# Kernel optimization log

Hardware: AMD Instinct MI355X
Metric: run time of the kernel (lower is better)

The kernel has to match this reference:

```python
import jax, jax.numpy as jnp
import numpy as np

B, S, E = 2, 2048, 1024
D_ATTN, H = 1024, 16
HD = D_ATTN // H
SCALE = 1.0 / np.sqrt(D_ATTN)
ROPE_BASE = 10000.0


def setup_inputs() -> dict:
    key = jax.random.key(0)
    ks = jax.random.split(key, 7)
    def w(k, shape, scale):
        return jax.random.normal(k, shape, dtype=jnp.float32) * scale
    return {
        "q": w(ks[0], (B, S, E), 1.0),
        "k": w(ks[1], (B, S, E), 1.0),
        "v": w(ks[2], (B, S, E), 1.0),
        "Wq": w(ks[3], (D_ATTN, E), E ** -0.5),
        "Wk": w(ks[4], (D_ATTN, E), E ** -0.5),
        "Wv": w(ks[5], (D_ATTN, E), E ** -0.5),
        "Wo": w(ks[6], (E, D_ATTN), D_ATTN ** -0.5),
    }


def _rope(x):
    # x: [B, H, S, HD]; interleaved-pair rotary embedding over the seq axis
    s, d = x.shape[2], x.shape[3]
    half = d // 2
    inv_freq = 1.0 / (ROPE_BASE ** (jnp.arange(half, dtype=jnp.float32) * 2.0 / d))
    ang = jnp.arange(s, dtype=jnp.float32)[:, None] * inv_freq[None, :]  # [S, half]
    cos, sin = jnp.cos(ang), jnp.sin(ang)
    xr = x.reshape(x.shape[:-1] + (half, 2))
    x0, x1 = xr[..., 0], xr[..., 1]
    o0 = x0 * cos - x1 * sin
    o1 = x0 * sin + x1 * cos
    return jnp.stack([o0, o1], axis=-1).reshape(x.shape)


def reference(q, k, v, Wq, Wk, Wv, Wo):
    # linear projections (nn.Linear with weight [out, in]): y = x @ W^T
    qh = (q @ Wq.T).reshape(B, S, H, HD).transpose(0, 2, 1, 3)  # [B,H,S,HD]
    kh = (k @ Wk.T).reshape(B, S, H, HD).transpose(0, 2, 1, 3)
    vh = (v @ Wv.T).reshape(B, S, H, HD).transpose(0, 2, 1, 3)
    qh = _rope(qh)
    kh = _rope(kh)
    # shifted-causal mask: disallow j >= i (diagonal masked), except (0,0) allowed
    i = jnp.arange(S)[:, None]
    j = jnp.arange(S)[None, :]
    masked = j >= i                              # triu incl. diagonal
    masked = masked.at[0, 0].set(False)          # keep (0,0) so row 0 isn't all -inf
    scores = jnp.einsum("bhsd,bhtd->bhst", qh, kh) * SCALE
    scores = jnp.where(masked, -jnp.inf, scores)
    probs = jax.nn.softmax(scores, axis=-1)      # dropout omitted (eval mode)
    ctx = jnp.einsum("bhst,bhtd->bhsd", probs, vh)
    ctx = ctx.transpose(0, 2, 1, 3).reshape(B, S, D_ATTN)
    return ctx @ Wo.T
```

## Files before the change

kernel.cpp:

```cpp
#include <hip/hip_runtime.h>
#include <hip/hip_bf16.h>

#define BATCH 2
#define SEQ   2048
#define EMB   1024
#define DATTN 1024
#define NH    16
#define HD    64
#define MM    (BATCH*SEQ)
#define SCALE 0.03125f
#define MINIT -1.0e30f
#define ROPE_COEF 0.41524101186f

using bf16x8 = __attribute__((ext_vector_type(8))) short;
using f32x4  = __attribute__((ext_vector_type(4))) float;

__device__ inline short f2bf(float x) {
    __hip_bfloat16 b = __float2bfloat16(x);
    return *reinterpret_cast<short*>(&b);
}

__device__ inline void gl_lds16(const short* g, short* l) {
    __builtin_amdgcn_global_load_lds(
        (const __attribute__((address_space(1))) unsigned int*)g,
        (__attribute__((address_space(3))) unsigned int*)l, 16, 0, 0);
}

__global__ __launch_bounds__(256)
void cvt_all(const float* __restrict__ q, const float* __restrict__ k,
             const float* __restrict__ v,
             const float* __restrict__ Wq, const float* __restrict__ Wk,
             const float* __restrict__ Wv, const float* __restrict__ Wo,
             short* __restrict__ dst)
{
    const long QKV = (long)MM * EMB;
    const long WSZ = (long)DATTN * EMB;
    const long i = ((long)blockIdx.x * 256 + threadIdx.x) * 4;
    const float* s;
    long off;
    if (i < 3 * QKV) {
        const int seg = (int)(i / QKV);
        off = i - (long)seg * QKV;
        s = (seg == 0) ? q : (seg == 1) ? k : v;
    } else {
        const long j = i - 3 * QKV;
        const int seg = (int)(j / WSZ);
        off = j - (long)seg * WSZ;
        s = (seg == 0) ? Wq : (seg == 1) ? Wk : (seg == 2) ? Wv : Wo;
    }
    float4 x = *(const float4*)(s + off);
    short4 y;
    y.x = f2bf(x.x); y.y = f2bf(x.y); y.z = f2bf(x.z); y.w = f2bf(x.w);
    *(short4*)(dst + i) = y;
}

__device__ inline void stage_tile64(const short* g, short* lds, int tid) {
    #pragma unroll
    for (int c = 0; c < 4; ++c) {
        const int cc   = c * 256 + tid;
        const int row  = cc >> 3;
        const int slot = cc & 7;
        const int ssl  = slot ^ (row & 7);
        gl_lds16(g + (long)row * EMB + ssl * 8, lds + ((cc & ~63) << 3));
    }
}

__device__ inline void stage_tile64h(const short* g, short* lds, int tid) {
    #pragma unroll
    for (int c = 0; c < 2; ++c) {
        const int cc   = c * 256 + tid;
        const int row  = cc >> 3;
        const int ssl  = (cc & 7) ^ (row & 7);
        gl_lds16(g + (long)row * EMB + ssl * 8, lds + ((cc & ~63) << 3));
    }
}

__global__ __launch_bounds__(256)
void gemm_proj_bf16(const short* __restrict__ qb, const short* __restrict__ kb,
                    const short* __restrict__ vb,
                    const short* __restrict__ wqb, const short* __restrict__ wkb,
                    const short* __restrict__ wvb,
                    short* __restrict__ Qb, short* __restrict__ Kb,
                    short* __restrict__ Vtb)
{
    const short* A; const short* B;
    if (blockIdx.z == 0)      { A = qb; B = wqb; }
    else if (blockIdx.z == 1) { A = kb; B = wkb; }
    else                      { A = vb; B = wvb; }
    const bool isv = (blockIdx.z == 2);

    __shared__ short sA[128 * 64];
    __shared__ short sB[128 * 64];

    const int tid  = threadIdx.x;
    const int wave = tid >> 6, lane = tid & 63;
    const int quad = lane >> 4, l16 = lane & 15;
    const int wm = (wave >> 1) * 64, wn = (wave & 1) * 64;
    const long m0 = (long)blockIdx.x * 128, n0 = (long)blockIdx.y * 128;
    const int rsw = l16 & 7;

    f32x4 acc[4][4];
    #pragma unroll
    for (int i = 0; i < 4; ++i)
        #pragma unroll
        for (int j = 0; j < 4; ++j) acc[i][j] = (f32x4){0.f, 0.f, 0.f, 0.f};

    for (int kt = 0; kt < EMB; kt += 64) {
        __syncthreads();
        stage_tile64(A + m0 * EMB + kt, sA, tid);
        stage_tile64(B + n0 * EMB + kt, sB, tid);
        __syncthreads();

        #pragma unroll
        for (int kk = 0; kk < 2; ++kk) {
            bf16x8 af[4], bfr[4];
            #pragma unroll
            for (int rt = 0; rt < 4; ++rt)
                af[rt] = *(const bf16x8*)&sA[(wm + rt * 16 + l16) * 64
                         + (((kk << 2) | quad) ^ rsw) * 8];
            #pragma unroll
            for (int ct = 0; ct < 4; ++ct)
                bfr[ct] = *(const bf16x8*)&sB[(wn + ct * 16 + l16) * 64
                          + (((kk << 2) | quad) ^ rsw) * 8];
            if (isv) {
                #pragma unroll
                for (int i = 0; i < 4; ++i)
                    #pragma unroll
                    for (int j = 0; j < 4; ++j)
                        acc[i][j] = __builtin_amdgcn_mfma_f32_16x16x32_bf16(
                            af[i], bfr[j], acc[i][j], 0, 0, 0);
            } else {
                #pragma unroll
                for (int i = 0; i < 4; ++i)
                    #pragma unroll
                    for (int j = 0; j < 4; ++j)
                        acc[i][j] = __builtin_amdgcn_mfma_f32_16x16x32_bf16(
                            bfr[i], af[j], acc[i][j], 0, 0, 0);
            }
        }
    }

    if (!isv) {
        short* C = (blockIdx.z == 0) ? Qb : Kb;
        const float scl = (blockIdx.z == 0) ? SCALE : 1.0f;
        #pragma unroll
        for (int i = 0; i < 4; ++i) {
            const int d0  = (int)(n0) + wn + i * 16 + quad * 4;
            const int hh  = d0 >> 6, dd0 = d0 & (HD - 1);
            const float invf0 = exp2f(-ROPE_COEF * (float)(dd0 >> 1));
            const float invf1 = exp2f(-ROPE_COEF * (float)((dd0 >> 1) + 1));
            #pragma unroll
            for (int j = 0; j < 4; ++j) {
                const int tok = (int)(m0) + wm + j * 16 + l16;
                const int bb = tok >> 11, ss = tok & (SEQ - 1);
                float s0, c0, s1, c1;
                __sincosf((float)ss * invf0, &s0, &c0);
                __sincosf((float)ss * invf1, &s1, &c1);
                const f32x4 x = acc[i][j];
                short4 o4;
                o4.x = f2bf((x[0] * c0 - x[1] * s0) * scl);
                o4.y = f2bf((x[0] * s0 + x[1] * c0) * scl);
                o4.z = f2bf((x[2] * c1 - x[3] * s1) * scl);
                o4.w = f2bf((x[2] * s1 + x[3] * c1) * scl);
                *(short4*)&C[(((long)(bb * NH + hh)) << 17)
                             + ((long)ss << 6) + dd0] = o4;
            }
        }
    } else {
        #pragma unroll
        for (int rt = 0; rt < 4; ++rt) {
            #pragma unroll
            for (int ct = 0; ct < 4; ++ct) {
                const long row0 = m0 + wm + rt * 16 + quad * 4;
                const long col  = n0 + wn + ct * 16 + l16;
                const int bb = (int)(row0 >> 11), ss = (int)(row0 & (SEQ - 1));
                const int hh = (int)(col >> 6),   dd = (int)(col & (HD - 1));
                short4 s4;
                s4.x = f2bf(acc[rt][ct][0]); s4.y = f2bf(acc[rt][ct][1]);
                s4.z = f2bf(acc[rt][ct][2]); s4.w = f2bf(acc[rt][ct][3]);
                *(short4*)&Vtb[(((long)(bb * NH + hh)) << 17) + ((long)dd << 11) + ss] = s4;
            }
        }
    }
}

__global__ __launch_bounds__(256)
void gemm_out_bf16(const short* __restrict__ Ab, const short* __restrict__ Bb,
                   float* __restrict__ C)
{
    __shared__ short sA[128 * 64];
    __shared__ short sB[64 * 64];

    const int tid  = threadIdx.x;
    const int wave = tid >> 6, lane = tid & 63;
    const int quad = lane >> 4, l16 = lane & 15;
    const int wm = (wave >> 1) * 64, wn = (wave & 1) * 32;
    const long m0 = (long)blockIdx.x * 128, n0 = (long)blockIdx.y * 64;
    const int rsw = l16 & 7;

    f32x4 acc[4][2];
    #pragma unroll
    for (int i = 0; i < 4; ++i)
        #pragma unroll
        for (int j = 0; j < 2; ++j) acc[i][j] = (f32x4){0.f, 0.f, 0.f, 0.f};

    for (int kt = 0; kt < DATTN; kt += 64) {
        __syncthreads();
        stage_tile64(Ab + m0 * DATTN + kt, sA, tid);
        stage_tile64h(Bb + n0 * DATTN + kt, sB, tid);
        __syncthreads();

        #pragma unroll
        for (int kk = 0; kk < 2; ++kk) {
            bf16x8 af[4], bfr[2];
            #pragma unroll
            for (int rt = 0; rt < 4; ++rt)
                af[rt] = *(const bf16x8*)&sA[(wm + rt * 16 + l16) * 64
                         + (((kk << 2) | quad) ^ rsw) * 8];
            #pragma unroll
            for (int ct = 0; ct < 2; ++ct)
                bfr[ct] = *(const bf16x8*)&sB[(wn + ct * 16 + l16) * 64
                          + (((kk << 2) | quad) ^ rsw) * 8];
            #pragma unroll
            for (int rt = 0; rt < 4; ++rt)
                #pragma unroll
                for (int ct = 0; ct < 2; ++ct)
                    acc[rt][ct] = __builtin_amdgcn_mfma_f32_16x16x32_bf16(
                        af[rt], bfr[ct], acc[rt][ct], 0, 0, 0);
        }
    }

    #pragma unroll
    for (int rt = 0; rt < 4; ++rt) {
        #pragma unroll
        for (int ct = 0; ct < 2; ++ct) {
            #pragma unroll
            for (int reg = 0; reg < 4; ++reg) {
                const long row = m0 + wm + rt * 16 + quad * 4 + reg;
                const long col = n0 + wn + ct * 16 + l16;
                C[row * EMB + col] = acc[rt][ct][reg];
            }
        }
    }
}

#define KLD 64
#define PLD 72

__device__ inline void stage_kv64(const short* __restrict__ Kb,
                                  const short* __restrict__ Vtb,
                                  long base, int jb2,
                                  short* skp, short* svp,
                                  int tid, int wave)
{
    #pragma unroll
    for (int c = 0; c < 2; ++c) {
        const int cc  = c * 256 + tid;
        const int row = cc >> 3;
        const int sch = (cc & 7) ^ (row & 7);
        short* dk = skp + ((c * 256 + (tid & ~63)) << 3) - ((tid & ~63) << 3)
                        + (((c * 256 + tid) & ~63) - (c * 256 + tid - (tid & 63)) ) ;
        (void)dk;
        gl_lds16(Kb + base + (long)(jb2 + row) * HD + sch * 8,
                 skp + ((c * 256 + wave * 64) << 3));
        gl_lds16(Vtb + base + ((long)row << 11) + jb2 + sch * 8,
                 svp + ((c * 256 + wave * 64) << 3));
    }
}

__global__ __launch_bounds__(256, 3)
void flash_attn_mfma(const short* __restrict__ Qb,
                     const short* __restrict__ Kb,
                     const short* __restrict__ Vtb,
                     short* __restrict__ ctx)
{
    const int id  = blockIdx.x;
    const int hi  = id >> 8;
    const int idx = id & 255;
    const int r   = idx & 7;
    const int s5  = idx >> 3;
    const int pi  = s5 & 3;
    const int ts8 = s5 >> 2;
    const int p   = r + 8 * pi;
    const int b   = p >> 4, h = p & 15;
    const int t   = hi ? ts8 : (15 - ts8);

    const int tid = threadIdx.x;
    const int wave = tid >> 6, lane = tid & 63;
    const int quad = lane >> 4, l16 = lane & 15;
    const int r0 = t * 128;

    __shared__ short sk[2][64 * KLD];
    __shared__ short sv[2][64 * KLD];
    __shared__ short sp[4][32 * PLD];

    const long base = ((long)(b * NH + h)) << 17;

    const int iq0 = r0 + wave * 32 + l16;
    const int iq1 = iq0 + 16;
    const int dtile = 2 * t + (wave >> 1);
    const int rsw = l16 & 7;

    bf16x8 qf0[2], qf1[2];
    #pragma unroll
    for (int tt = 0; tt < 2; ++tt) {
        qf0[tt] = *(const bf16x8*)(Qb + base + (long)iq0 * HD + tt * 32 + quad * 8);
        qf1[tt] = *(const bf16x8*)(Qb + base + (long)iq1 * HD + tt * 32 + quad * 8);
    }

    f32x4 acc0[4], acc1[4];
    #pragma unroll
    for (int ct = 0; ct < 4; ++ct) {
        acc0[ct] = (f32x4){0.f, 0.f, 0.f, 0.f};
        acc1[ct] = (f32x4){0.f, 0.f, 0.f, 0.f};
    }
    float m0 = MINIT, l0 = 0.f;
    float m1 = MINIT, l1 = 0.f;

    const int J = 2 * t + 2;

    stage_kv64(Kb, Vtb, base, 0, sk[0], sv[0], tid, wave);

    #pragma unroll 1
    for (int j2 = 0; j2 < J; ++j2) {
        const int pb = j2 & 1;
        asm volatile("s_waitcnt vmcnt(0)" ::: "memory");
        __builtin_amdgcn_s_barrier();
        if (j2 + 1 < J)
            stage_kv64(Kb, Vtb, base, (j2 + 1) * 64,
                       sk[pb ^ 1], sv[pb ^ 1], tid, wave);

        if (j2 <= dtile) {
            const int jb2 = j2 * 64;
            const short* skh = sk[pb];
            const short* svh = sv[pb];

            f32x4 s0[4], s1[4];
            __builtin_amdgcn_s_setprio(1);
            #pragma unroll
            for (int ct = 0; ct < 4; ++ct) {
                const int rr16 = (ct * 16 + l16) * KLD;
                bf16x8 k0 = *(const bf16x8*)&skh[rr16 + ((quad ^ rsw) << 3)];
                bf16x8 k1 = *(const bf16x8*)&skh[rr16 + (((4 + quad) ^ rsw) << 3)];
                f32x4 z0 = (f32x4){0.f, 0.f, 0.f, 0.f};
                z0 = __builtin_amdgcn_mfma_f32_16x16x32_bf16(k0, qf0[0], z0, 0, 0, 0);
                z0 = __builtin_amdgcn_mfma_f32_16x16x32_bf16(k1, qf0[1], z0, 0, 0, 0);
                s0[ct] = z0;
                f32x4 z1 = (f32x4){0.f, 0.f, 0.f, 0.f};
                z1 = __builtin_amdgcn_mfma_f32_16x16x32_bf16(k0, qf1[0], z1, 0, 0, 0);
                z1 = __builtin_amdgcn_mfma_f32_16x16x32_bf16(k1, qf1[1], z1, 0, 0, 0);
                s1[ct] = z1;
            }
            __builtin_amdgcn_s_setprio(0);

            if (j2 == dtile) {
                #pragma unroll
                for (int ct = 0; ct < 4; ++ct)
                    #pragma unroll
                    for (int rr = 0; rr < 4; ++rr) {
                        const int j = jb2 + ct * 16 + quad * 4 + rr;
                        if (!((j < iq0) || (iq0 == 0 && j == 0)))
                            s0[ct][rr] = -INFINITY;
                        if (!(j < iq1))
                            s1[ct][rr] = -INFINITY;
                    }
            }

            float mx0 = MINIT;
            #pragma unroll
            for (int ct = 0; ct < 4; ++ct)
                #pragma unroll
                for (int rr = 0; rr < 4; ++rr) mx0 = fmaxf(mx0, s0[ct][rr]);
            mx0 = fmaxf(mx0, __shfl_xor(mx0, 16, 64));
            mx0 = fmaxf(mx0, __shfl_xor(mx0, 32, 64));
            const float mn0 = fmaxf(m0, mx0);
            const float a0 = __expf(m0 - mn0);
            m0 = mn0;
            float ss0 = 0.f;
            #pragma unroll
            for (int ct = 0; ct < 4; ++ct)
                #pragma unroll
                for (int rr = 0; rr < 4; ++rr) {
                    const float e = __expf(s0[ct][rr] - mn0);
                    s0[ct][rr] = e;
                    ss0 += e;
                }
            ss0 += __shfl_xor(ss0, 16, 64);
            ss0 += __shfl_xor(ss0, 32, 64);
            l0 = l0 * a0 + ss0;

            float mx1 = MINIT;
            #pragma unroll
            for (int ct = 0; ct < 4; ++ct)
                #pragma unroll
                for (int rr = 0; rr < 4; ++rr) mx1 = fmaxf(mx1, s1[ct][rr]);
            mx1 = fmaxf(mx1, __shfl_xor(mx1, 16, 64));
            mx1 = fmaxf(mx1, __shfl_xor(mx1, 32, 64));
            const float mn1 = fmaxf(m1, mx1);
            const float a1 = __expf(m1 - mn1);
            m1 = mn1;
            float ss1 = 0.f;
            #pragma unroll
            for (int ct = 0; ct < 4; ++ct)
                #pragma unroll
                for (int rr = 0; rr < 4; ++rr) {
                    const float e = __expf(s1[ct][rr] - mn1);
                    s1[ct][rr] = e;
                    ss1 += e;
                }
            ss1 += __shfl_xor(ss1, 16, 64);
            ss1 += __shfl_xor(ss1, 32, 64);
            l1 = l1 * a1 + ss1;

            short* pw0 = sp[wave];
            short* pw1 = sp[wave] + 16 * PLD;
            #pragma unroll
            for (int ct = 0; ct < 4; ++ct) {
                short4 p4;
                p4.x = f2bf(s0[ct][0]); p4.y = f2bf(s0[ct][1]);
                p4.z = f2bf(s0[ct][2]); p4.w = f2bf(s0[ct][3]);
                *(short4*)&pw0[l16 * PLD + ct * 16 + quad * 4] = p4;
                short4 q4;
                q4.x = f2bf(s1[ct][0]); q4.y = f2bf(s1[ct][1]);
                q4.z = f2bf(s1[ct][2]); q4.w = f2bf(s1[ct][3]);
                *(short4*)&pw1[l16 * PLD + ct * 16 + quad * 4] = q4;
            }

            #pragma unroll
            for (int ct = 0; ct < 4; ++ct)
                #pragma unroll
                for (int rr = 0; rr < 4; ++rr) {
                    acc0[ct][rr] *= a0;
                    acc1[ct][rr] *= a1;
                }

            bf16x8 pf00 = *(const bf16x8*)&pw0[l16 * PLD + quad * 8];
            bf16x8 pf01 = *(const bf16x8*)&pw0[l16 * PLD + 32 + quad * 8];
            bf16x8 pf10 = *(const bf16x8*)&pw1[l16 * PLD + quad * 8];
            bf16x8 pf11 = *(const bf16x8*)&pw1[l16 * PLD + 32 + quad * 8];

            __builtin_amdgcn_s_setprio(1);
            #pragma unroll
            for (int ct = 0; ct < 4; ++ct) {
                const int rr16 = (ct * 16 + l16) * KLD;
                bf16x8 v0 = *(const bf16x8*)&svh[rr16 + ((quad ^ rsw) << 3)];
                bf16x8 v1 = *(const bf16x8*)&svh[rr16 + (((4 + quad) ^ rsw) << 3)];
                acc0[ct] = __builtin_amdgcn_mfma_f32_16x16x32_bf16(
                    v0, pf00, acc0[ct], 0, 0, 0);
                acc0[ct] = __builtin_amdgcn_mfma_f32_16x16x32_bf16(
                    v1, pf01, acc0[ct], 0, 0, 0);
                acc1[ct] = __builtin_amdgcn_mfma_f32_16x16x32_bf16(
                    v0, pf10, acc1[ct], 0, 0, 0);
                acc1[ct] = __builtin_amdgcn_mfma_f32_16x16x32_bf16(
                    v1, pf11, acc1[ct], 0, 0, 0);
            }
            __builtin_amdgcn_s_setprio(0);
        }
    }

    {
        const float inv0 = 1.f / l0;
        short* orow = ctx + (long)(b * SEQ + iq0) * DATTN + h * HD;
        #pragma unroll
        for (int ct = 0; ct < 4; ++ct) {
            short4 o4;
            o4.x = f2bf(acc0[ct][0] * inv0);
            o4.y = f2bf(acc0[ct][1] * inv0);
            o4.z = f2bf(acc0[ct][2] * inv0);
            o4.w = f2bf(acc0[ct][3] * inv0);
            *(short4*)&orow[ct * 16 + quad * 4] = o4;
        }
    }
    {
        const float inv1 = 1.f / l1;
        short* orow = ctx + (long)(b * SEQ + iq1) * DATTN + h * HD;
        #pragma unroll
        for (int ct = 0; ct < 4; ++ct) {
            short4 o4;
            o4.x = f2bf(acc1[ct][0] * inv1);
            o4.y = f2bf(acc1[ct][1] * inv1);
            o4.z = f2bf(acc1[ct][2] * inv1);
            o4.w = f2bf(acc1[ct][3] * inv1);
            *(short4*)&orow[ct * 16 + quad * 4] = o4;
        }
    }
}

extern "C" void kernel_launch(void* const* d_in, const int* in_sizes, int n_in,
                              void* d_out, int out_size, void* d_ws, size_t ws_size,
                              hipStream_t stream) {
    const float* q  = (const float*)d_in[0];
    const float* k  = (const float*)d_in[1];
    const float* v  = (const float*)d_in[2];
    const float* Wq = (const float*)d_in[3];
    const float* Wk = (const float*)d_in[4];
    const float* Wv = (const float*)d_in[5];
    const float* Wo = (const float*)d_in[6];
    float* out = (float*)d_out;

    const long QKV = (long)MM * EMB;
    const long WSZ = (long)DATTN * EMB;
    short* basep = (short*)d_ws;
    short* qb  = basep;
    short* kb  = qb + QKV;
    short* vb  = kb + QKV;
    short* wqb = vb + QKV;
    short* wkb = wqb + WSZ;
    short* wvb = wkb + WSZ;
    short* wob = wvb + WSZ;
    short* Qb  = wob + WSZ;
    short* Kb  = Qb + QKV;
    short* Vtb = Kb + QKV;
    short* ctx = Vtb + QKV;

    cvt_all<<<16384, 256, 0, stream>>>(q, k, v, Wq, Wk, Wv, Wo, qb);

    gemm_proj_bf16<<<dim3(MM / 128, DATTN / 128, 3), 256, 0, stream>>>(
        qb, kb, vb, wqb, wkb, wvb, Qb, Kb, Vtb);

    flash_attn_mfma<<<512, 256, 0, stream>>>(Qb, Kb, Vtb, ctx);

    gemm_out_bf16<<<dim3(MM / 128, EMB / 64), 256, 0, stream>>>(ctx, wob, out);
}
```

Baseline: 211.0 us.

## Load K/V straight to registers in flash attention with smaller 64-row blocks

The flash-attention kernel no longer stages K and V tiles through double-buffered shared memory with barriers. Each wave now loads its K/V MFMA fragments directly from global memory into registers. Blocks shrink to 128 threads covering 64 query rows, and the grid doubles to 1024 with a new load-balancing order for causal tile lengths. This removes LDS staging and block-wide barriers, and the finer grid should balance the causal workload better. In exchange, both waves of a block fetch the same K/V from global memory or L2 with no reuse, and the loads are no longer prefetched a tile ahead.

```diff
diff --git a/kernel.cpp b/kernel.cpp
--- a/kernel.cpp
+++ b/kernel.cpp
@@ -244,62 +244,38 @@
     }
 }
 
-#define KLD 64
 #define PLD 72
 
-__device__ inline void stage_kv64(const short* __restrict__ Kb,
-                                  const short* __restrict__ Vtb,
-                                  long base, int jb2,
-                                  short* skp, short* svp,
-                                  int tid, int wave)
-{
-    #pragma unroll
-    for (int c = 0; c < 2; ++c) {
-        const int cc  = c * 256 + tid;
-        const int row = cc >> 3;
-        const int sch = (cc & 7) ^ (row & 7);
-        short* dk = skp + ((c * 256 + (tid & ~63)) << 3) - ((tid & ~63) << 3)
-                        + (((c * 256 + tid) & ~63) - (c * 256 + tid - (tid & 63)) ) ;
-        (void)dk;
-        gl_lds16(Kb + base + (long)(jb2 + row) * HD + sch * 8,
-                 skp + ((c * 256 + wave * 64) << 3));
-        gl_lds16(Vtb + base + ((long)row << 11) + jb2 + sch * 8,
-                 svp + ((c * 256 + wave * 64) << 3));
-    }
-}
-
-__global__ __launch_bounds__(256, 3)
+__global__ __launch_bounds__(128, 2)
 void flash_attn_mfma(const short* __restrict__ Qb,
                      const short* __restrict__ Kb,
                      const short* __restrict__ Vtb,
                      short* __restrict__ ctx)
 {
-    const int id  = blockIdx.x;
-    const int hi  = id >> 8;
-    const int idx = id & 255;
-    const int r   = idx & 7;
-    const int s5  = idx >> 3;
-    const int pi  = s5 & 3;
-    const int ts8 = s5 >> 2;
-    const int p   = r + 8 * pi;
-    const int b   = p >> 4, h = p & 15;
-    const int t   = hi ? ts8 : (15 - ts8);
-
-    const int tid = threadIdx.x;
+    const int id = blockIdx.x;
+    const int r  = id & 7;
+    const int pi = (id >> 3) & 3;
+    const int us = id >> 5;
+    const int p  = r + 8 * pi;
+    const int b  = p >> 4, h = p & 15;
+    int u;
+    if      (us < 8)  u = 31 - us;
+    else if (us < 16) u = us - 8;
+    else if (us < 24) u = 39 - us;
+    else              u = us - 16;
+
+    const int tid  = threadIdx.x;
     const int wave = tid >> 6, lane = tid & 63;
     const int quad = lane >> 4, l16 = lane & 15;
-    const int r0 = t * 128;
-
-    __shared__ short sk[2][64 * KLD];
-    __shared__ short sv[2][64 * KLD];
-    __shared__ short sp[4][32 * PLD];
+
+    __shared__ short sp[2][32 * PLD];
 
     const long base = ((long)(b * NH + h)) << 17;
-
-    const int iq0 = r0 + wave * 32 + l16;
+    const short* __restrict__ kb = Kb + base;
+    const short* __restrict__ vb = Vtb + base;
+
+    const int iq0 = u * 64 + wave * 32 + l16;
     const int iq1 = iq0 + 16;
-    const int dtile = 2 * t + (wave >> 1);
-    const int rsw = l16 & 7;
 
     bf16x8 qf0[2], qf1[2];
     #pragma unroll
@@ -317,145 +293,137 @@
     float m0 = MINIT, l0 = 0.f;
     float m1 = MINIT, l1 = 0.f;
 
-    const int J = 2 * t + 2;
-
-    stage_kv64(Kb, Vtb, base, 0, sk[0], sv[0], tid, wave);
+    const int J = u + 1;
 
     #pragma unroll 1
     for (int j2 = 0; j2 < J; ++j2) {
-        const int pb = j2 & 1;
-        asm volatile("s_waitcnt vmcnt(0)" ::: "memory");
-        __builtin_amdgcn_s_barrier();
-        if (j2 + 1 < J)
-            stage_kv64(Kb, Vtb, base, (j2 + 1) * 64,
-                       sk[pb ^ 1], sv[pb ^ 1], tid, wave);
-
-        if (j2 <= dtile) {
-            const int jb2 = j2 * 64;
-            const short* skh = sk[pb];
-            const short* svh = sv[pb];
-
-            f32x4 s0[4], s1[4];
-            __builtin_amdgcn_s_setprio(1);
-            #pragma unroll
-            for (int ct = 0; ct < 4; ++ct) {
-                const int rr16 = (ct * 16 + l16) * KLD;
-                bf16x8 k0 = *(const bf16x8*)&skh[rr16 + ((quad ^ rsw) << 3)];
-                bf16x8 k1 = *(const bf16x8*)&skh[rr16 + (((4 + quad) ^ rsw) << 3)];
-                f32x4 z0 = (f32x4){0.f, 0.f, 0.f, 0.f};
-                z0 = __builtin_amdgcn_mfma_f32_16x16x32_bf16(k0, qf0[0], z0, 0, 0, 0);
-                z0 = __builtin_amdgcn_mfma_f32_16x16x32_bf16(k1, qf0[1], z0, 0, 0, 0);
-                s0[ct] = z0;
-                f32x4 z1 = (f32x4){0.f, 0.f, 0.f, 0.f};
-                z1 = __builtin_amdgcn_mfma_f32_16x16x32_bf16(k0, qf1[0], z1, 0, 0, 0);
-                z1 = __builtin_amdgcn_mfma_f32_16x16x32_bf16(k1, qf1[1], z1, 0, 0, 0);
-                s1[ct] = z1;
-            }
-            __builtin_amdgcn_s_setprio(0);
-
-            if (j2 == dtile) {
-                #pragma unroll
-                for (int ct = 0; ct < 4; ++ct)
-                    #pragma unroll
-                    for (int rr = 0; rr < 4; ++rr) {
-                        const int j = jb2 + ct * 16 + quad * 4 + rr;
-                        if (!((j < iq0) || (iq0 == 0 && j == 0)))
-                            s0[ct][rr] = -INFINITY;
-                        if (!(j < iq1))
-                            s1[ct][rr] = -INFINITY;
-                    }
-            }
-
-            float mx0 = MINIT;
-            #pragma unroll
-            for (int ct = 0; ct < 4; ++ct)
-                #pragma unroll
-                for (int rr = 0; rr < 4; ++rr) mx0 = fmaxf(mx0, s0[ct][rr]);
-            mx0 = fmaxf(mx0, __shfl_xor(mx0, 16, 64));
-            mx0 = fmaxf(mx0, __shfl_xor(mx0, 32, 64));
-            const float mn0 = fmaxf(m0, mx0);
-            const float a0 = __expf(m0 - mn0);
-            m0 = mn0;
-            float ss0 = 0.f;
+        const int jb2 = j2 * 64;
+
+        bf16x8 kf0[4], kf1[4], vf0[4], vf1[4];
+        #pragma unroll
+        for (int ct = 0; ct < 4; ++ct) {
+            const long krow = (long)(jb2 + ct * 16 + l16) * HD + quad * 8;
+            kf0[ct] = *(const bf16x8*)(kb + krow);
+            kf1[ct] = *(const bf16x8*)(kb + krow + 32);
+            const long vrow = ((long)(ct * 16 + l16) << 11) + jb2 + quad * 8;
+            vf0[ct] = *(const bf16x8*)(vb + vrow);
+            vf1[ct] = *(const bf16x8*)(vb + vrow + 32);
+        }
+
+        f32x4 s0[4], s1[4];
+        __builtin_amdgcn_s_setprio(1);
+        #pragma unroll
+        for (int ct = 0; ct < 4; ++ct) {
+            f32x4 z0 = (f32x4){0.f, 0.f, 0.f, 0.f};
+            z0 = __builtin_amdgcn_mfma_f32_16x16x32_bf16(kf0[ct], qf0[0], z0, 0, 0, 0);
+            z0 = __builtin_amdgcn_mfma_f32_16x16x32_bf16(kf1[ct], qf0[1], z0, 0, 0, 0);
+            s0[ct] = z0;
+            f32x4 z1 = (f32x4){0.f, 0.f, 0.f, 0.f};
+            z1 = __builtin_amdgcn_mfma_f32_16x16x32_bf16(kf0[ct], qf1[0], z1, 0, 0, 0);
+            z1 = __builtin_amdgcn_mfma_f32_16x16x32_bf16(kf1[ct], qf1[1], z1, 0, 0, 0);
+            s1[ct] = z1;
+        }
+        __builtin_amdgcn_s_setprio(0);
+
+        if (j2 == u) {
             #pragma unroll
             for (int ct = 0; ct < 4; ++ct)
                 #pragma unroll
                 for (int rr = 0; rr < 4; ++rr) {
-                    const float e = __expf(s0[ct][rr] - mn0);
-                    s0[ct][rr] = e;
-                    ss0 += e;
+                    const int j = jb2 + ct * 16 + quad * 4 + rr;
+                    if (!((j < iq0) || (iq0 == 0 && j == 0)))
+                        s0[ct][rr] = -INFINITY;
+                    if (!(j < iq1))
+                        s1[ct][rr] = -INFINITY;
                 }
-            ss0 += __shfl_xor(ss0, 16, 64);
-            ss0 += __shfl_xor(ss0, 32, 64);
-            l0 = l0 * a0 + ss0;
-
-            float mx1 = MINIT;
-            #pragma unroll
-            for (int ct = 0; ct < 4; ++ct)
-                #pragma unroll
-                for (int rr = 0; rr < 4; ++rr) mx1 = fmaxf(mx1, s1[ct][rr]);
-            mx1 = fmaxf(mx1, __shfl_xor(mx1, 16, 64));
-            mx1 = fmaxf(mx1, __shfl_xor(mx1, 32, 64));
-            const float mn1 = fmaxf(m1, mx1);
-            const float a1 = __expf(m1 - mn1);
-            m1 = mn1;
-            float ss1 = 0.f;
-            #pragma unroll
-            for (int ct = 0; ct < 4; ++ct)
-                #pragma unroll
-                for (int rr = 0; rr < 4; ++rr) {
-                    const float e = __expf(s1[ct][rr] - mn1);
-                    s1[ct][rr] = e;
-                    ss1 += e;
-                }
-            ss1 += __shfl_xor(ss1, 16, 64);
-            ss1 += __shfl_xor(ss1, 32, 64);
-            l1 = l1 * a1 + ss1;
-
-            short* pw0 = sp[wave];
-            short* pw1 = sp[wave] + 16 * PLD;
-            #pragma unroll
-            for (int ct = 0; ct < 4; ++ct) {
-                short4 p4;
-                p4.x = f2bf(s0[ct][0]); p4.y = f2bf(s0[ct][1]);
-                p4.z = f2bf(s0[ct][2]); p4.w = f2bf(s0[ct][3]);
-                *(short4*)&pw0[l16 * PLD + ct * 16 + quad * 4] = p4;
-                short4 q4;
-                q4.x = f2bf(s1[ct][0]); q4.y = f2bf(s1[ct][1]);
-                q4.z = f2bf(s1[ct][2]); q4.w = f2bf(s1[ct][3]);
-                *(short4*)&pw1[l16 * PLD + ct * 16 + quad * 4] = q4;
-            }
-
-            #pragma unroll
-            for (int ct = 0; ct < 4; ++ct)
-                #pragma unroll
-                for (int rr = 0; rr < 4; ++rr) {
-                    acc0[ct][rr] *= a0;
-                    acc1[ct][rr] *= a1;
-                }
-
-            bf16x8 pf00 = *(const bf16x8*)&pw0[l16 * PLD + quad * 8];
-            bf16x8 pf01 = *(const bf16x8*)&pw0[l16 * PLD + 32 + quad * 8];
-            bf16x8 pf10 = *(const bf16x8*)&pw1[l16 * PLD + quad * 8];
-            bf16x8 pf11 = *(const bf16x8*)&pw1[l16 * PLD + 32 + quad * 8];
-
-            __builtin_amdgcn_s_setprio(1);
-            #pragma unroll
-            for (int ct = 0; ct < 4; ++ct) {
-                const int rr16 = (ct * 16 + l16) * KLD;
-                bf16x8 v0 = *(const bf16x8*)&svh[rr16 + ((quad ^ rsw) << 3)];
-                bf16x8 v1 = *(const bf16x8*)&svh[rr16 + (((4 + quad) ^ rsw) << 3)];
-                acc0[ct] = __builtin_amdgcn_mfma_f32_16x16x32_bf16(
-                    v0, pf00, acc0[ct], 0, 0, 0);
-                acc0[ct] = __builtin_amdgcn_mfma_f32_16x16x32_bf16(
-                    v1, pf01, acc0[ct], 0, 0, 0);
-                acc1[ct] = __builtin_amdgcn_mfma_f32_16x16x32_bf16(
-                    v0, pf10, acc1[ct], 0, 0, 0);
-                acc1[ct] = __builtin_amdgcn_mfma_f32_16x16x32_bf16(
-                    v1, pf11, acc1[ct], 0, 0, 0);
-            }
-            __builtin_amdgcn_s_setprio(0);
-        }
+        }
+
+        float mx0 = MINIT;
+        #pragma unroll
+        for (int ct = 0; ct < 4; ++ct)
+            #pragma unroll
+            for (int rr = 0; rr < 4; ++rr) mx0 = fmaxf(mx0, s0[ct][rr]);
+        mx0 = fmaxf(mx0, __shfl_xor(mx0, 16, 64));
+        mx0 = fmaxf(mx0, __shfl_xor(mx0, 32, 64));
+        const float mn0 = fmaxf(m0, mx0);
+        const float a0 = __expf(m0 - mn0);
+        m0 = mn0;
+        float ss0 = 0.f;
+        #pragma unroll
+        for (int ct = 0; ct < 4; ++ct)
+            #pragma unroll
+            for (int rr = 0; rr < 4; ++rr) {
+                const float e = __expf(s0[ct][rr] - mn0);
+                s0[ct][rr] = e;
+                ss0 += e;
+            }
+        ss0 += __shfl_xor(ss0, 16, 64);
+        ss0 += __shfl_xor(ss0, 32, 64);
+        l0 = l0 * a0 + ss0;
+
+        float mx1 = MINIT;
+        #pragma unroll
+        for (int ct = 0; ct < 4; ++ct)
+            #pragma unroll
+            for (int rr = 0; rr < 4; ++rr) mx1 = fmaxf(mx1, s1[ct][rr]);
+        mx1 = fmaxf(mx1, __shfl_xor(mx1, 16, 64));
+        mx1 = fmaxf(mx1, __shfl_xor(mx1, 32, 64));
+        const float mn1 = fmaxf(m1, mx1);
+        const float a1 = __expf(m1 - mn1);
+        m1 = mn1;
+        float ss1 = 0.f;
+        #pragma unroll
+        for (int ct = 0; ct < 4; ++ct)
+            #pragma unroll
+            for (int rr = 0; rr < 4; ++rr) {
+                const float e = __expf(s1[ct][rr] - mn1);
+                s1[ct][rr] = e;
+                ss1 += e;
+            }
+        ss1 += __shfl_xor(ss1, 16, 64);
+        ss1 += __shfl_xor(ss1, 32, 64);
+        l1 = l1 * a1 + ss1;
+
+        short* pw0 = sp[wave];
+        short* pw1 = sp[wave] + 16 * PLD;
+        #pragma unroll
+        for (int ct = 0; ct < 4; ++ct) {
+            short4 p4;
+            p4.x = f2bf(s0[ct][0]); p4.y = f2bf(s0[ct][1]);
+            p4.z = f2bf(s0[ct][2]); p4.w = f2bf(s0[ct][3]);
+            *(short4*)&pw0[l16 * PLD + ct * 16 + quad * 4] = p4;
+            short4 q4;
+            q4.x = f2bf(s1[ct][0]); q4.y = f2bf(s1[ct][1]);
+            q4.z = f2bf(s1[ct][2]); q4.w = f2bf(s1[ct][3]);
+            *(short4*)&pw1[l16 * PLD + ct * 16 + quad * 4] = q4;
+        }
+
+        #pragma unroll
+        for (int ct = 0; ct < 4; ++ct)
+            #pragma unroll
+            for (int rr = 0; rr < 4; ++rr) {
+                acc0[ct][rr] *= a0;
+                acc1[ct][rr] *= a1;
+            }
+
+        bf16x8 pf00 = *(const bf16x8*)&pw0[l16 * PLD + quad * 8];
+        bf16x8 pf01 = *(const bf16x8*)&pw0[l16 * PLD + 32 + quad * 8];
+        bf16x8 pf10 = *(const bf16x8*)&pw1[l16 * PLD + quad * 8];
+        bf16x8 pf11 = *(const bf16x8*)&pw1[l16 * PLD + 32 + quad * 8];
+
+        __builtin_amdgcn_s_setprio(1);
+        #pragma unroll
+        for (int ct = 0; ct < 4; ++ct) {
+            acc0[ct] = __builtin_amdgcn_mfma_f32_16x16x32_bf16(
+                vf0[ct], pf00, acc0[ct], 0, 0, 0);
+            acc0[ct] = __builtin_amdgcn_mfma_f32_16x16x32_bf16(
+                vf1[ct], pf01, acc0[ct], 0, 0, 0);
+            acc1[ct] = __builtin_amdgcn_mfma_f32_16x16x32_bf16(
+                vf0[ct], pf10, acc1[ct], 0, 0, 0);
+            acc1[ct] = __builtin_amdgcn_mfma_f32_16x16x32_bf16(
+                vf1[ct], pf11, acc1[ct], 0, 0, 0);
+        }
+        __builtin_amdgcn_s_setprio(0);
     }
 
     {
@@ -518,7 +486,7 @@
     gemm_proj_bf16<<<dim3(MM / 128, DATTN / 128, 3), 256, 0, stream>>>(
         qb, kb, vb, wqb, wkb, wvb, Qb, Kb, Vtb);
 
-    flash_attn_mfma<<<512, 256, 0, stream>>>(Qb, Kb, Vtb, ctx);
+    flash_attn_mfma<<<1024, 128, 0, stream>>>(Qb, Kb, Vtb, ctx);
 
     gemm_out_bf16<<<dim3(MM / 128, EMB / 64), 256, 0, stream>>>(ctx, wob, out);
 }
```

Result: slower. 230.7 us (+9.3%).

## Use 128-wide KV tiles, exp2 softmax with folded log2e scale, lazy rescale

Applied to the files above, without the earlier changes.

Replaces the double-buffered 64-key KV staging loop with single-buffered 128-key tiles loaded synchronously between two barriers. Every wave now processes the same tiles (no per-wave diagonal skip), halving the loop trips. Log2(e) is folded into the Q scale so softmax can use exp2f, and the accumulator rescale is skipped when no row max grows. Occupancy drops to 2 blocks per CU, and without double buffering the global-to-LDS load latency is no longer overlapped with compute.

```diff
diff --git a/kernel.cpp b/kernel.cpp
--- a/kernel.cpp
+++ b/kernel.cpp
@@ -9,6 +9,7 @@
 #define HD    64
 #define MM    (BATCH*SEQ)
 #define SCALE 0.03125f
+#define QSCALE 0.0450842200278f
 #define MINIT -1.0e30f
 #define ROPE_COEF 0.41524101186f
 
@@ -142,7 +143,7 @@
 
     if (!isv) {
         short* C = (blockIdx.z == 0) ? Qb : Kb;
-        const float scl = (blockIdx.z == 0) ? SCALE : 1.0f;
+        const float scl = (blockIdx.z == 0) ? QSCALE : 1.0f;
         #pragma unroll
         for (int i = 0; i < 4; ++i) {
             const int d0  = (int)(n0) + wn + i * 16 + quad * 4;
@@ -247,28 +248,7 @@
 #define KLD 64
 #define PLD 72
 
-__device__ inline void stage_kv64(const short* __restrict__ Kb,
-                                  const short* __restrict__ Vtb,
-                                  long base, int jb2,
-                                  short* skp, short* svp,
-                                  int tid, int wave)
-{
-    #pragma unroll
-    for (int c = 0; c < 2; ++c) {
-        const int cc  = c * 256 + tid;
-        const int row = cc >> 3;
-        const int sch = (cc & 7) ^ (row & 7);
-        short* dk = skp + ((c * 256 + (tid & ~63)) << 3) - ((tid & ~63) << 3)
-                        + (((c * 256 + tid) & ~63) - (c * 256 + tid - (tid & 63)) ) ;
-        (void)dk;
-        gl_lds16(Kb + base + (long)(jb2 + row) * HD + sch * 8,
-                 skp + ((c * 256 + wave * 64) << 3));
-        gl_lds16(Vtb + base + ((long)row << 11) + jb2 + sch * 8,
-                 svp + ((c * 256 + wave * 64) << 3));
-    }
-}
-
-__global__ __launch_bounds__(256, 3)
+__global__ __launch_bounds__(256, 2)
 void flash_attn_mfma(const short* __restrict__ Qb,
                      const short* __restrict__ Kb,
                      const short* __restrict__ Vtb,
@@ -290,15 +270,14 @@
     const int quad = lane >> 4, l16 = lane & 15;
     const int r0 = t * 128;
 
-    __shared__ short sk[2][64 * KLD];
-    __shared__ short sv[2][64 * KLD];
+    __shared__ short sk[128 * KLD];
+    __shared__ short sv[128 * KLD];
     __shared__ short sp[4][32 * PLD];
 
     const long base = ((long)(b * NH + h)) << 17;
 
     const int iq0 = r0 + wave * 32 + l16;
     const int iq1 = iq0 + 16;
-    const int dtile = 2 * t + (wave >> 1);
     const int rsw = l16 & 7;
 
     bf16x8 qf0[2], qf1[2];
@@ -317,128 +296,142 @@
     float m0 = MINIT, l0 = 0.f;
     float m1 = MINIT, l1 = 0.f;
 
-    const int J = 2 * t + 2;
-
-    stage_kv64(Kb, Vtb, base, 0, sk[0], sv[0], tid, wave);
-
     #pragma unroll 1
-    for (int j2 = 0; j2 < J; ++j2) {
-        const int pb = j2 & 1;
-        asm volatile("s_waitcnt vmcnt(0)" ::: "memory");
-        __builtin_amdgcn_s_barrier();
-        if (j2 + 1 < J)
-            stage_kv64(Kb, Vtb, base, (j2 + 1) * 64,
-                       sk[pb ^ 1], sv[pb ^ 1], tid, wave);
-
-        if (j2 <= dtile) {
-            const int jb2 = j2 * 64;
-            const short* skh = sk[pb];
-            const short* svh = sv[pb];
-
-            f32x4 s0[4], s1[4];
-            __builtin_amdgcn_s_setprio(1);
-            #pragma unroll
-            for (int ct = 0; ct < 4; ++ct) {
-                const int rr16 = (ct * 16 + l16) * KLD;
-                bf16x8 k0 = *(const bf16x8*)&skh[rr16 + ((quad ^ rsw) << 3)];
-                bf16x8 k1 = *(const bf16x8*)&skh[rr16 + (((4 + quad) ^ rsw) << 3)];
-                f32x4 z0 = (f32x4){0.f, 0.f, 0.f, 0.f};
-                z0 = __builtin_amdgcn_mfma_f32_16x16x32_bf16(k0, qf0[0], z0, 0, 0, 0);
-                z0 = __builtin_amdgcn_mfma_f32_16x16x32_bf16(k1, qf0[1], z0, 0, 0, 0);
-                s0[ct] = z0;
-                f32x4 z1 = (f32x4){0.f, 0.f, 0.f, 0.f};
-                z1 = __builtin_amdgcn_mfma_f32_16x16x32_bf16(k0, qf1[0], z1, 0, 0, 0);
-                z1 = __builtin_amdgcn_mfma_f32_16x16x32_bf16(k1, qf1[1], z1, 0, 0, 0);
-                s1[ct] = z1;
-            }
-            __builtin_amdgcn_s_setprio(0);
-
-            if (j2 == dtile) {
+    for (int jt = 0; jt <= t; ++jt) {
+        const int jbase = jt * 128;
+
+        __syncthreads();
+        #pragma unroll
+        for (int c = 0; c < 4; ++c) {
+            const int cc  = c * 256 + tid;
+            const int row = cc >> 3;
+            const int sch = (cc & 7) ^ (row & 7);
+            gl_lds16(Kb + base + (long)(jbase + row) * HD + sch * 8,
+                     sk + ((c * 256 + wave * 64) << 3));
+            const int vrow = row & 63, vh = cc >> 9;
+            gl_lds16(Vtb + base + ((long)vrow << 11) + jbase + vh * 64 + sch * 8,
+                     sv + ((c * 256 + wave * 64) << 3));
+        }
+        __syncthreads();
+
+        f32x4 s0[8], s1[8];
+        __builtin_amdgcn_s_setprio(1);
+        #pragma unroll
+        for (int g = 0; g < 8; ++g) {
+            const int rr16 = (g * 16 + l16) * KLD;
+            bf16x8 k0 = *(const bf16x8*)&sk[rr16 + ((quad ^ rsw) << 3)];
+            bf16x8 k1 = *(const bf16x8*)&sk[rr16 + (((4 + quad) ^ rsw) << 3)];
+            f32x4 z0 = (f32x4){0.f, 0.f, 0.f, 0.f};
+            z0 = __builtin_amdgcn_mfma_f32_16x16x32_bf16(k0, qf0[0], z0, 0, 0, 0);
+            z0 = __builtin_amdgcn_mfma_f32_16x16x32_bf16(k1, qf0[1], z0, 0, 0, 0);
+            s0[g] = z0;
+            f32x4 z1 = (f32x4){0.f, 0.f, 0.f, 0.f};
+            z1 = __builtin_amdgcn_mfma_f32_16x16x32_bf16(k0, qf1[0], z1, 0, 0, 0);
+            z1 = __builtin_amdgcn_mfma_f32_16x16x32_bf16(k1, qf1[1], z1, 0, 0, 0);
+            s1[g] = z1;
+        }
+        __builtin_amdgcn_s_setprio(0);
+
+        if (jt == t) {
+            #pragma unroll
+            for (int g = 0; g < 8; ++g)
                 #pragma unroll
-                for (int ct = 0; ct < 4; ++ct)
-                    #pragma unroll
-                    for (int rr = 0; rr < 4; ++rr) {
-                        const int j = jb2 + ct * 16 + quad * 4 + rr;
-                        if (!((j < iq0) || (iq0 == 0 && j == 0)))
-                            s0[ct][rr] = -INFINITY;
-                        if (!(j < iq1))
-                            s1[ct][rr] = -INFINITY;
-                    }
-            }
-
-            float mx0 = MINIT;
+                for (int rr = 0; rr < 4; ++rr) {
+                    const int j = jbase + g * 16 + quad * 4 + rr;
+                    if (!((j < iq0) || (iq0 == 0 && j == 0)))
+                        s0[g][rr] = -INFINITY;
+                    if (!(j < iq1))
+                        s1[g][rr] = -INFINITY;
+                }
+        }
+
+        float mx0 = MINIT;
+        #pragma unroll
+        for (int g = 0; g < 8; ++g)
+            #pragma unroll
+            for (int rr = 0; rr < 4; ++rr) mx0 = fmaxf(mx0, s0[g][rr]);
+        mx0 = fmaxf(mx0, __shfl_xor(mx0, 16, 64));
+        mx0 = fmaxf(mx0, __shfl_xor(mx0, 32, 64));
+        const float mo0 = m0;
+        const float mn0 = fmaxf(mo0, mx0);
+        m0 = mn0;
+        float ss0 = 0.f;
+        #pragma unroll
+        for (int g = 0; g < 8; ++g)
+            #pragma unroll
+            for (int rr = 0; rr < 4; ++rr) {
+                const float e = exp2f(s0[g][rr] - mn0);
+                s0[g][rr] = e;
+                ss0 += e;
+            }
+        ss0 += __shfl_xor(ss0, 16, 64);
+        ss0 += __shfl_xor(ss0, 32, 64);
+        if (__any(mx0 > mo0)) {
+            const float a0 = exp2f(mo0 - mn0);
             #pragma unroll
             for (int ct = 0; ct < 4; ++ct)
                 #pragma unroll
-                for (int rr = 0; rr < 4; ++rr) mx0 = fmaxf(mx0, s0[ct][rr]);
-            mx0 = fmaxf(mx0, __shfl_xor(mx0, 16, 64));
-            mx0 = fmaxf(mx0, __shfl_xor(mx0, 32, 64));
-            const float mn0 = fmaxf(m0, mx0);
-            const float a0 = __expf(m0 - mn0);
-            m0 = mn0;
-            float ss0 = 0.f;
+                for (int rr = 0; rr < 4; ++rr) acc0[ct][rr] *= a0;
+            l0 = l0 * a0 + ss0;
+        } else {
+            l0 += ss0;
+        }
+
+        float mx1 = MINIT;
+        #pragma unroll
+        for (int g = 0; g < 8; ++g)
+            #pragma unroll
+            for (int rr = 0; rr < 4; ++rr) mx1 = fmaxf(mx1, s1[g][rr]);
+        mx1 = fmaxf(mx1, __shfl_xor(mx1, 16, 64));
+        mx1 = fmaxf(mx1, __shfl_xor(mx1, 32, 64));
+        const float mo1 = m1;
+        const float mn1 = fmaxf(mo1, mx1);
+        m1 = mn1;
+        float ss1 = 0.f;
+        #pragma unroll
+        for (int g = 0; g < 8; ++g)
+            #pragma unroll
+            for (int rr = 0; rr < 4; ++rr) {
+                const float e = exp2f(s1[g][rr] - mn1);
+                s1[g][rr] = e;
+                ss1 += e;
+            }
+        ss1 += __shfl_xor(ss1, 16, 64);
+        ss1 += __shfl_xor(ss1, 32, 64);
+        if (__any(mx1 > mo1)) {
+            const float a1 = exp2f(mo1 - mn1);
             #pragma unroll
             for (int ct = 0; ct < 4; ++ct)
                 #pragma unroll
-                for (int rr = 0; rr < 4; ++rr) {
-                    const float e = __expf(s0[ct][rr] - mn0);
-                    s0[ct][rr] = e;
-                    ss0 += e;
-                }
-            ss0 += __shfl_xor(ss0, 16, 64);
-            ss0 += __shfl_xor(ss0, 32, 64);
-            l0 = l0 * a0 + ss0;
-
-            float mx1 = MINIT;
-            #pragma unroll
-            for (int ct = 0; ct < 4; ++ct)
-                #pragma unroll
-                for (int rr = 0; rr < 4; ++rr) mx1 = fmaxf(mx1, s1[ct][rr]);
-            mx1 = fmaxf(mx1, __shfl_xor(mx1, 16, 64));
-            mx1 = fmaxf(mx1, __shfl_xor(mx1, 32, 64));
-            const float mn1 = fmaxf(m1, mx1);
-            const float a1 = __expf(m1 - mn1);
-            m1 = mn1;
-            float ss1 = 0.f;
-            #pragma unroll
-            for (int ct = 0; ct < 4; ++ct)
-                #pragma unroll
-                for (int rr = 0; rr < 4; ++rr) {
-                    const float e = __expf(s1[ct][rr] - mn1);
-                    s1[ct][rr] = e;
-                    ss1 += e;
-                }
-            ss1 += __shfl_xor(ss1, 16, 64);
-            ss1 += __shfl_xor(ss1, 32, 64);
+                for (int rr = 0; rr < 4; ++rr) acc1[ct][rr] *= a1;
             l1 = l1 * a1 + ss1;
-
-            short* pw0 = sp[wave];
-            short* pw1 = sp[wave] + 16 * PLD;
-            #pragma unroll
-            for (int ct = 0; ct < 4; ++ct) {
+        } else {
+            l1 += ss1;
+        }
+
+        short* pw0 = sp[wave];
+        short* pw1 = sp[wave] + 16 * PLD;
+        #pragma unroll
+        for (int hf = 0; hf < 2; ++hf) {
+            #pragma unroll
+            for (int c2 = 0; c2 < 4; ++c2) {
+                const int g = hf * 4 + c2;
                 short4 p4;
-                p4.x = f2bf(s0[ct][0]); p4.y = f2bf(s0[ct][1]);
-                p4.z = f2bf(s0[ct][2]); p4.w = f2bf(s0[ct][3]);
-                *(short4*)&pw0[l16 * PLD + ct * 16 + quad * 4] = p4;
+                p4.x = f2bf(s0[g][0]); p4.y = f2bf(s0[g][1]);
+                p4.z = f2bf(s0[g][2]); p4.w = f2bf(s0[g][3]);
+                *(short4*)&pw0[l16 * PLD + c2 * 16 + quad * 4] = p4;
                 short4 q4;
-                q4.x = f2bf(s1[ct][0]); q4.y = f2bf(s1[ct][1]);
-                q4.z = f2bf(s1[ct][2]); q4.w = f2bf(s1[ct][3]);
-                *(short4*)&pw1[l16 * PLD + ct * 16 + quad * 4] = q4;
-            }
-
-            #pragma unroll
-            for (int ct = 0; ct < 4; ++ct)
-                #pragma unroll
-                for (int rr = 0; rr < 4; ++rr) {
-                    acc0[ct][rr] *= a0;
-                    acc1[ct][rr] *= a1;
-                }
+                q4.x = f2bf(s1[g][0]); q4.y = f2bf(s1[g][1]);
+                q4.z = f2bf(s1[g][2]); q4.w = f2bf(s1[g][3]);
+                *(short4*)&pw1[l16 * PLD + c2 * 16 + quad * 4] = q4;
+            }
 
             bf16x8 pf00 = *(const bf16x8*)&pw0[l16 * PLD + quad * 8];
             bf16x8 pf01 = *(const bf16x8*)&pw0[l16 * PLD + 32 + quad * 8];
             bf16x8 pf10 = *(const bf16x8*)&pw1[l16 * PLD + quad * 8];
             bf16x8 pf11 = *(const bf16x8*)&pw1[l16 * PLD + 32 + quad * 8];
 
+            const short* svh = sv + hf * 64 * KLD;
             __builtin_amdgcn_s_setprio(1);
             #pragma unroll
             for (int ct = 0; ct < 4; ++ct) {
```

After: 219.9 us. +4.2%, slower.
